# Kernel optimization log

Measured on AMD Instinct MI355X. Metric: run time of the kernel, lower is better.

## Reference

```python
import jax, jax.numpy as jnp
import numpy as np

N_HEADS = 4
N_CLASS = 20
REL_PATTERN = [(5, 3)]
DIF_PATTERN = [(3, 6)]


def im2col(x, ksize, dilation):
    # x: (N,C,H,W) -> (C, ksize*ksize, H*W*N); last dim flattened in (h,w,n) order,
    # matching the torch im2col_indices / permute(1,2,3,0) layout used by the module.
    N, C, H, W = x.shape
    p = (ksize // 2) * dilation
    xp = jnp.pad(x, ((0, 0), (0, 0), (p, p), (p, p)))
    cols = jnp.stack([xp[:, :, fi * dilation:fi * dilation + H, fj * dilation:fj * dilation + W]
                      for fi in range(ksize) for fj in range(ksize)], axis=2)  # (N,C,K2,H,W)
    return cols.transpose(1, 2, 3, 4, 0).reshape(C, ksize * ksize, H * W * N)


def col2im(cols, shape, ksize, dilation):
    # cols: (C*K2, H*W*N) -> scatter-add back to (N,C,H,W) (inverse of im2col).
    N, C, H, W = shape
    p = (ksize // 2) * dilation
    K2 = ksize * ksize
    c = cols.reshape(C, K2, H, W, N).transpose(4, 0, 1, 2, 3)  # (N,C,K2,H,W)
    out = jnp.zeros((N, C, H + 2 * p, W + 2 * p), cols.dtype)
    k = 0
    for fi in range(ksize):
        for fj in range(ksize):
            out = out.at[:, :, fi * dilation:fi * dilation + H, fj * dilation:fj * dilation + W].add(c[:, :, k])
            k += 1
    return out[:, :, p:p + H, p:p + W]


def gap_pred(x, w):
    hm = jnp.einsum('nchw,kc->nhwk', x, w)  # heatmaps
    return hm.reshape(x.shape[0], -1, hm.shape[-1]).mean(1), hm


def make_mask(heatmaps, label):
    N, H, W, _ = heatmaps.shape
    sm = jax.nn.relu(heatmaps)
    m = jnp.take_along_axis(sm, label[:, None, None, None], axis=3)[..., 0]  # (N,H,W)
    mx = jnp.clip(m.reshape(N, -1).max(1), 1.0, None)
    return jax.lax.stop_gradient((m / mx[:, None, None])[:, None])  # (N,1,H,W), detached


def infusion(V, Kc, Qc, ksize, dilation, n_heads):
    N, Dv, H, W = V.shape
    D = Kc.shape[1]
    h_dim, vh_dim, K2 = D // n_heads, Dv // n_heads, ksize * ksize
    L = H * W * N
    Kt = im2col(Kc, ksize, dilation).reshape(n_heads, h_dim, K2, L)
    Qt = Qc.transpose(1, 2, 3, 0).reshape(n_heads, h_dim, L)
    att = jax.nn.softmax(jnp.einsum('ahkl,ahl->akl', Kt, Qt), axis=1)  # softmax over window
    Vt = im2col(V, ksize, dilation).reshape(n_heads, vh_dim, K2, L)
    out = jnp.einsum('avkl,akl->avl', Vt, att).reshape(Dv, H, W, N)
    return out.transpose(3, 0, 1, 2)


def diffusion(V, Kc, Qc, ksize, dilation, mask, n_heads):
    N, Dv, H, W = V.shape
    D = Kc.shape[1]
    h_dim, vh_dim, K2 = D // n_heads, Dv // n_heads, ksize * ksize
    L = H * W * N
    Kt = im2col(Kc, ksize, dilation).reshape(n_heads, h_dim, K2, L)
    Qt = Qc.transpose(1, 2, 3, 0).reshape(n_heads, h_dim, L)
    att = jax.nn.softmax(jnp.einsum('ahkl,ahl->akl', Kt, Qt), axis=1)
    mflat = mask[:, 0].transpose(1, 2, 0).reshape(-1)  # (H*W*N)
    att = att * mflat[None, None, :]
    Vt = V.transpose(1, 2, 3, 0).reshape(n_heads, vh_dim, L)
    Vcols = (Vt[:, :, None, :] * att[:, None, :, :]).reshape(Dv * K2, L)
    return col2im(Vcols, V.shape, ksize, dilation)


def setup_inputs() -> dict:
    key = jax.random.key(0)
    ks = jax.random.split(key, 8)
    N, C, H, W = 4, 256, 64, 64
    return {
        'feats': jax.random.normal(ks[0], (N, C, H, W), jnp.float32),
        'K': jax.random.normal(ks[1], (N, C, H, W), jnp.float32),
        'Q': jax.random.normal(ks[2], (N, C, H, W), jnp.float32),
        'w_gap': jax.random.normal(ks[3], (N_CLASS, C), jnp.float32) * 0.05,
        'w_gap_r': jax.random.normal(ks[4], (N_CLASS, C), jnp.float32) * 0.05,
        'conv_w': jax.random.normal(ks[5], (C, 2 * C, 3, 3), jnp.float32) * 0.02,
        'conv_b': jax.random.normal(ks[6], (C,), jnp.float32) * 0.02,
        'label': jax.random.randint(ks[7], (N,), 0, N_CLASS),
    }


def reference(feats, K, Q, w_gap, w_gap_r, conv_w, conv_b, label):
    pred, hm = gap_pred(feats, w_gap)
    mask = make_mask(hm, label)
    # NOTE: Bayes calls infuse(feats, Q, K, ...) with K/Q swapped vs the Infusion signature.
    feats_r = sum(infusion(feats, Q, K, ksz, dil, N_HEADS) for ksz, dil in REL_PATTERN)
    pred_r, _ = gap_pred(feats_r, w_gap_r)
    feats_d = sum(diffusion(feats, K, Q, ksz, dil, mask, N_HEADS) for ksz, dil in DIF_PATTERN)
    x = jnp.concatenate([feats * mask, feats_d], axis=1)
    nxt = jax.lax.conv_general_dilated(x, conv_w, (1, 1), ((1, 1), (1, 1)),
                                       dimension_numbers=('NCHW', 'OIHW', 'NCHW'))
    nxt = nxt + conv_b[None, :, None, None]
    return nxt, pred, pred_r
```

## Files before the change

kernel.cpp:

```cpp
#include <hip/hip_runtime.h>
#include <hip/hip_bf16.h>

#define N_IMG 4
#define C_CH 256
#define H_DIM 64
#define W_DIM 64
#define HW 4096
#define NCLASS 20
#define NHEADS 4
#define HD 64

typedef __attribute__((ext_vector_type(8))) short short8;
typedef __attribute__((ext_vector_type(4))) float f32x4;

__device__ __forceinline__ ushort f2bf(float f) {
    unsigned u = __float_as_uint(f);
    u += 0x7FFFu + ((u >> 16) & 1u);
    return (ushort)(u >> 16);
}

__global__ __launch_bounds__(256) void k_phaseA(
    ushort* __restrict__ xinp,
    const float* __restrict__ feats, const float* __restrict__ wgap,
    const int* __restrict__ label,
    float* __restrict__ mask, unsigned* __restrict__ mmax,
    float* __restrict__ S_f,
    const float* __restrict__ patch_t,
    const float* __restrict__ center_t,
    float* __restrict__ att_inf,
    const float* __restrict__ cw, ushort* __restrict__ wt3) {
    __shared__ __align__(16) float smem[1600];
    int b = blockIdx.x;
    int t = threadIdx.x;

    if (b < 1040) {
        int n = b / 260, seg = b % 260;
        size_t base;
        if (seg < 66)       base = ((size_t)(n * 66 + 0) * 66 + seg) * 512;
        else if (seg < 132) base = ((size_t)(n * 66 + 65) * 66 + (seg - 66)) * 512;
        else {
            int c = seg - 132;
            int r = 1 + (c >> 1), x = (c & 1) ? 65 : 0;
            base = ((size_t)(n * 66 + r) * 66 + x) * 512;
        }
        ((unsigned*)(xinp + base))[t] = 0u;
    } else if (b < 1296) {
        int bb = b - 1040;
        int n = bb >> 6, h = bb & 63;
        int w = t & 63, cq = t >> 6;
        float* wrow = smem;
        float* part = smem + 256;
        int lab = label[n];
        wrow[t] = wgap[lab * C_CH + t];
        __syncthreads();
        const float* fp = feats + ((size_t)(n * C_CH + cq * 64)) * HW + h * W_DIM + w;
        float acc = 0.f;
        for (int c = 0; c < 64; c++) acc += fp[(size_t)c * HW] * wrow[cq * 64 + c];
        part[cq * 64 + w] = acc;
        __syncthreads();
        if (cq == 0) {
            float m = fmaxf(part[w] + part[64 + w] + part[128 + w] + part[192 + w], 0.f);
            mask[n * HW + h * W_DIM + w] = m;
            for (int off = 32; off; off >>= 1) m = fmaxf(m, __shfl_down(m, off, 64));
            if (w == 0) atomicMax(&mmax[n], __float_as_uint(m));
        }
    } else if (b < 2320) {
        int nc = b - 1296;
        const float* p = feats + (size_t)nc * HW;
        float s = 0.f;
        for (int i = t; i < HW; i += 256) s += p[i];
        float* red = smem;
        for (int off = 32; off; off >>= 1) s += __shfl_down(s, off, 64);
        int wid = t >> 6;
        if ((t & 63) == 0) red[wid] = s;
        __syncthreads();
        if (t == 0) S_f[nc] = red[0] + red[1] + red[2] + red[3];
    } else if (b < 3344) {
        int idx = b - 2320;
        int a = idx >> 8;
        int bb = idx & 255;
        int n = bb >> 6, h = bb & 63;
        int w = t & 63;
        int kq = t >> 6;
        float* att_s = smem;

        int k0 = (kq == 0) ? 0 : (1 + kq * 6);
        int nk = (kq == 0) ? 7 : 6;
        int offc[7]; float msk[7];
#pragma unroll
        for (int j = 0; j < 7; j++) {
            int k = k0 + ((j < nk) ? j : 0);
            int y = h + (k / 5 - 2) * 3, x = w + (k % 5 - 2) * 3;
            bool v = (y >= 0 && y < 64 && x >= 0 && x < 64) && (j < nk);
            offc[j] = v ? y * 64 + x : 0;
            msk[j] = v ? 1.f : 0.f;
        }
        float s[7];
#pragma unroll
        for (int j = 0; j < 7; j++) s[j] = 0.f;
        const float* cp = center_t + ((size_t)(n * C_CH + a * HD)) * HW + h * W_DIM + w;
        const float* pp = patch_t + ((size_t)(n * C_CH + a * HD)) * HW;
        for (int c4 = 0; c4 < 64; c4 += 4) {
            float cen[4];
            float pv[4][7];
#pragma unroll
            for (int u = 0; u < 4; u++)
                cen[u] = cp[(size_t)(c4 + u) * HW];
#pragma unroll
            for (int u = 0; u < 4; u++) {
                const float* pc = pp + (size_t)(c4 + u) * HW;
#pragma unroll
                for (int j = 0; j < 7; j++)
                    if (j < nk) pv[u][j] = pc[offc[j]];
            }
#pragma unroll
            for (int u = 0; u < 4; u++)
#pragma unroll
                for (int j = 0; j < 7; j++)
                    if (j < nk) s[j] += pv[u][j] * msk[j] * cen[u];
        }
#pragma unroll
        for (int j = 0; j < 7; j++)
            if (j < nk) att_s[(k0 + j) * 64 + w] = s[j];
        __syncthreads();
        if (t < 64) {
            float v[25];
            float mx = -1e30f;
#pragma unroll
            for (int k = 0; k < 25; k++) { v[k] = att_s[k * 64 + t]; mx = fmaxf(mx, v[k]); }
            float sum = 0.f;
#pragma unroll
            for (int k = 0; k < 25; k++) { v[k] = __expf(v[k] - mx); sum += v[k]; }
            float inv = 1.0f / sum;
#pragma unroll
            for (int k = 0; k < 25; k++)
                att_inf[((size_t)(a * 25 + k) * N_IMG + n) * HW + h * 64 + t] = v[k] * inv;
        }
    } else {
        int idx = (b - 3344) * 256 + t;
        const float* p = cw + (size_t)idx * 9;
        int ic = idx & 511;
        int oc = idx >> 9;
        int icc = ic >> 5, lq = (ic & 31) >> 3, pos = ic & 7;
#pragma unroll
        for (int kk = 0; kk < 9; kk++)
            wt3[((((size_t)(icc * 9 + kk)) * 4 + lq) * 256 + oc) * 8 + pos] = f2bf(p[kk]);
    }
}

__global__ __launch_bounds__(1024) void k_phaseB(
    const float* __restrict__ patch_t,
    const float* __restrict__ center_t,
    const float* __restrict__ mask, const unsigned* __restrict__ mmax,
    float* __restrict__ att_dif,
    const float* __restrict__ att_inf, float* __restrict__ Wpl) {
    __shared__ float att_s[4][9][64];
    int b = blockIdx.x;
    int t = threadIdx.x;

    if (b < 256) {
        int n = b >> 6, h = b & 63;
        int w = t & 63;
        int a = (t >> 6) & 3;
        int cq = t >> 8;
        for (int i = t; i < 4 * 9 * 64; i += 1024) ((float*)att_s)[i] = 0.f;
        __syncthreads();
        int off[9];
#pragma unroll
        for (int k = 0; k < 9; k++) {
            int y = h + (k / 3 - 1) * 6, x = w + (k % 3 - 1) * 6;
            off[k] = (y >= 0 && y < 64 && x >= 0 && x < 64) ? y * 64 + x : -1;
        }
        float s[9];
#pragma unroll
        for (int k = 0; k < 9; k++) s[k] = 0.f;
        const float* cp = center_t + ((size_t)(n * C_CH + a * HD + cq * 16)) * HW + h * W_DIM + w;
        const float* pp = patch_t + ((size_t)(n * C_CH + a * HD + cq * 16)) * HW;
        for (int c = 0; c < 16; c++) {
            float cen = cp[(size_t)c * HW];
            const float* pc = pp + (size_t)c * HW;
#pragma unroll
            for (int k = 0; k < 9; k++) {
                float pv = (off[k] >= 0) ? pc[off[k]] : 0.f;
                s[k] += pv * cen;
            }
        }
#pragma unroll
        for (int k = 0; k < 9; k++) atomicAdd(&att_s[a][k][w], s[k]);
        __syncthreads();
        if (cq == 0) {
            float v[9];
            float mx = -1e30f;
#pragma unroll
            for (int k = 0; k < 9; k++) { v[k] = att_s[a][k][w]; mx = fmaxf(mx, v[k]); }
            float sum = 0.f;
#pragma unroll
            for (int k = 0; k < 9; k++) { v[k] = __expf(v[k] - mx); sum += v[k]; }
            float mnorm = fmaxf(__uint_as_float(mmax[n]), 1.0f);
            float mm = (mask[n * HW + h * W_DIM + w] / mnorm) / sum;
#pragma unroll
            for (int k = 0; k < 9; k++)
                att_dif[((size_t)(a * 9 + k) * N_IMG + n) * HW + h * W_DIM + w] = v[k] * mm;
        }
    } else {
        int b2 = b - 256;
        int x = t & 63, a = (t >> 6) & 3, yl = t >> 8;
        int row = b2 * 4 + yl;
        int n = row >> 6, y = row & 63;
        float s = 0.f;
#pragma unroll
        for (int k = 0; k < 25; k++) {
            int sy = y - (k / 5 - 2) * 3, sx = x - (k % 5 - 2) * 3;
            if (sy >= 0 && sy < 64 && sx >= 0 && sx < 64)
                s += att_inf[((size_t)(a * 25 + k) * N_IMG + n) * HW + sy * 64 + sx];
        }
        Wpl[((size_t)a * N_IMG + n) * HW + y * 64 + x] = s;
    }
}

__global__ __launch_bounds__(256) void k_phaseC(
    const float* __restrict__ feats, const float* __restrict__ Wpl,
    float* __restrict__ S_r,
    const float* __restrict__ mask, const unsigned* __restrict__ mmax,
    const float* __restrict__ att, ushort* __restrict__ xinp) {
    __shared__ __align__(16) char smemc[31488];
    int b = blockIdx.x;
    int t = threadIdx.x;

    if (b < 1024) {
        int nc = b;
        int n = nc >> 8, c = nc & 255;
        int a = c >> 6;
        const f32x4* p4 = (const f32x4*)(feats + (size_t)nc * HW);
        const f32x4* w4 = (const f32x4*)(Wpl + ((size_t)a * N_IMG + n) * HW);
        f32x4 a4 = (f32x4){0.f, 0.f, 0.f, 0.f};
        for (int i = t; i < HW / 4; i += 256) {
            f32x4 u = p4[i], v = w4[i];
            a4 += u * v;
        }
        float s = a4[0] + a4[1] + a4[2] + a4[3];
        float* red = (float*)smemc;
        for (int off = 32; off; off >>= 1) s += __shfl_down(s, off, 64);
        int wid = t >> 6;
        if ((t & 63) == 0) red[wid] = s;
        __syncthreads();
        if (t == 0) S_r[nc] = red[0] + red[1] + red[2] + red[3];
    } else {
        int idx = b - 1024;
        int y = idx & 63, n = (idx >> 6) & 3, g = idx >> 8;
        int x = t & 63, cg = t >> 6;
        float (*ftile)[32][64] = (float(*)[32][64])smemc;
        float (*att_s)[64]     = (float(*)[64])(smemc + 24576);
        ushort (*sx)[36]       = (ushort(*)[36])(smemc + 26880);
        short8 pk;
        if (g < 8) {
            int cbase = g * 32 + cg * 8;
            float mnorm = fmaxf(__uint_as_float(mmax[n]), 1.0f);
            float mval = mask[n * HW + y * 64 + x] / mnorm;
            const float* fp = feats + ((size_t)(n * C_CH + cbase)) * HW + y * 64 + x;
            float v[8];
#pragma unroll
            for (int i = 0; i < 8; i++) v[i] = fp[(size_t)i * HW];
#pragma unroll
            for (int i = 0; i < 8; i++) pk[i] = (short)f2bf(v[i] * mval);
        } else {
            int gd = g - 8;
            int a = gd >> 1;
            int cd = gd * 32;
            for (int idx2 = t; idx2 < 9 * 64; idx2 += 256) {
                int k = idx2 >> 6, w = idx2 & 63;
                int sy = y - (k / 3 - 1) * 6;
                att_s[k][w] = (sy >= 0 && sy < 64)
                    ? att[((size_t)(a * 9 + k) * N_IMG + n) * HW + sy * 64 + w] : 0.f;
            }
            const float* fb = feats + ((size_t)(n * C_CH + cd)) * HW;
#pragma unroll
            for (int i = 0; i < 24; i++) {
                int idx2 = t + 256 * i;
                int r = idx2 >> 11, c = (idx2 >> 6) & 31, xx = idx2 & 63;
                int ry = y + (r - 1) * 6;
                ((float*)ftile)[idx2] = (ry >= 0 && ry < 64)
                    ? fb[(size_t)c * HW + ry * 64 + xx] : 0.f;
            }
            __syncthreads();
#pragma unroll
            for (int cl = 0; cl < 8; cl++) {
                int c = cg * 8 + cl;
                float v = 0.f;
#pragma unroll
                for (int k = 0; k < 9; k++) {
                    int sxk = x - (k % 3 - 1) * 6;
                    if (sxk >= 0 && sxk < 64)
                        v += ftile[2 - k / 3][c][sxk] * att_s[k][sxk];
                }
                pk[cl] = (short)f2bf(v);
            }
        }
        __syncthreads();
        *(short8*)&sx[x][cg * 8] = pk;
        __syncthreads();
        int px = t >> 2, j = t & 3;
        short8 v8 = *(const short8*)&sx[px][j * 8];
        int chb = (g < 8) ? g * 32 : 256 + (g - 8) * 32;
        *(short8*)(xinp + ((size_t)((n * 66 + y + 1) * 66 + px + 1)) * 512 + chb + j * 8) = v8;
    }
}

#define LDS_PXW 32
__global__ __launch_bounds__(512, 4) void k_conv_mfma(
    const ushort* __restrict__ xinp,
    const ushort* __restrict__ wt3,
    const float* __restrict__ cb,
    float* __restrict__ out,
    const float* __restrict__ S_f, const float* __restrict__ wg,
    const float* __restrict__ S_r, const float* __restrict__ wgr,
    float* __restrict__ pred_out) {
    int bid = blockIdx.x;
    if (bid == 512) {
        int idx = threadIdx.x;
        if (idx < N_IMG * NCLASS) {
            int n = idx / NCLASS, k = idx % NCLASS;
            float s = 0.f;
            for (int c = 0; c < C_CH; c++) s += wg[k * C_CH + c] * S_f[n * C_CH + c];
            pred_out[idx] = s * (1.0f / HW);
        } else if (idx < 2 * N_IMG * NCLASS) {
            int j = idx - N_IMG * NCLASS;
            int n = j / NCLASS, k = j % NCLASS;
            float s = 0.f;
            for (int c = 0; c < C_CH; c++) s += wgr[k * C_CH + c] * S_r[n * C_CH + c];
            pred_out[idx] = s * (1.0f / HW);
        }
        return;
    }
    int t512 = threadIdx.x;
    int half = t512 >> 8;
    int th   = t512 & 255;
    int lane = t512 & 63;
    int wid  = (t512 >> 6) & 3;
    int w   = (bid & 7) * 64 + (bid >> 3);
    int och = w & 1;
    int y0  = (w >> 1) & 63;
    int n   = w >> 7;
    int ocw = och * 128 + wid * 32;
    int l15 = lane & 15, lq = lane >> 4;

    __shared__ ushort lds[2][2][792 * 8];

    f32x4 acc[2][4];
#pragma unroll
    for (int m = 0; m < 2; m++)
#pragma unroll
        for (int xs = 0; xs < 4; xs++) acc[m][xs] = (f32x4){0.f, 0.f, 0.f, 0.f};

    int s0 = th, s1 = th + 256, s2 = th + 512, s3 = th + 768;
    short8 g0, g1, g2, g3;
    int icb = half * 8;

#define SWZ_OFF(R, PX, J) (((((((R) * 66 + (PX)) << 2) | (J)) ^ ((PX) & 7)) << 3))

#define STAGE_LOAD(ICC)                                                              \
    {                                                                                \
        int icc_ = (ICC);                                                            \
        { int r = s0 / 264, rem = s0 % 264, px = rem >> 2, j = rem & 3;              \
          g0 = *(const short8*)(xinp + ((size_t)((n * 66 + y0 + r) * 66 + px)) * 512 \
                                 + icc_ * 32 + j * 8); }                             \
        { int r = s1 / 264, rem = s1 % 264, px = rem >> 2, j = rem & 3;              \
          g1 = *(const short8*)(xinp + ((size_t)((n * 66 + y0 + r) * 66 + px)) * 512 \
                                 + icc_ * 32 + j * 8); }                             \
        { int r = s2 / 264, rem = s2 % 264, px = rem >> 2, j = rem & 3;              \
          g2 = *(const short8*)(xinp + ((size_t)((n * 66 + y0 + r) * 66 + px)) * 512 \
                                 + icc_ * 32 + j * 8); }                             \
        if (s3 < 792) {                                                              \
          int r = s3 / 264, rem = s3 % 264, px = rem >> 2, j = rem & 3;              \
          g3 = *(const short8*)(xinp + ((size_t)((n * 66 + y0 + r) * 66 + px)) * 512 \
                                 + icc_ * 32 + j * 8); }                             \
    }

#define STAGE_WRITE(BUF)                                                             \
    {                                                                                \
        ushort* lb = &lds[half][BUF][0];                                             \
        { int r = s0 / 264, rem = s0 % 264, px = rem >> 2, j = rem & 3;              \
          *(short8*)&lb[SWZ_OFF(r, px, j)] = g0; }                                   \
        { int r = s1 / 264, rem = s1 % 264, px = rem >> 2, j = rem & 3;              \
          *(short8*)&lb[SWZ_OFF(r, px, j)] = g1; }                                   \
        { int r = s2 / 264, rem = s2 % 264, px = rem >> 2, j = rem & 3;              \
          *(short8*)&lb[SWZ_OFF(r, px, j)] = g2; }                                   \
        if (s3 < 792) {                                                              \
          int r = s3 / 264, rem = s3 % 264, px = rem >> 2, j = rem & 3;              \
          *(short8*)&lb[SWZ_OFF(r, px, j)] = g3; }                                   \
    }

    STAGE_LOAD(icb);
    STAGE_WRITE(0);
    __syncthreads();

    int cur = 0;
    for (int it = 0; it < 8; it++) {
        int icc = icb + it;
        if (it < 7) STAGE_LOAD(icc + 1);
        const ushort* lp = &lds[half][cur][0];
        const ushort* am0 = wt3 + (size_t)icc * 73728 + lq * 2048 + (ocw + l15) * 8;
        const ushort* am1 = am0 + 128;
        short8 a0c = *(const short8*)(am0);
        short8 a1c = *(const short8*)(am1);
        short8 a0n = *(const short8*)(am0 + 8192);
        short8 a1n = *(const short8*)(am1 + 8192);
#pragma unroll
        for (int kk = 0; kk < 9; kk++) {
            short8 a0nn, a1nn;
            if (kk < 7) {
                a0nn = *(const short8*)(am0 + (kk + 2) * 8192);
                a1nn = *(const short8*)(am1 + (kk + 2) * 8192);
            }
            int ky = kk / 3, kx = kk % 3;
            int kxl = kx + l15;
            const ushort* lrow = lp + SWZ_OFF(ky, kxl, lq);
            short8 b0 = *(const short8*)(lrow);
            short8 b1 = *(const short8*)(lrow + 16 * LDS_PXW);
            short8 b2 = *(const short8*)(lrow + 32 * LDS_PXW);
            short8 b3 = *(const short8*)(lrow + 48 * LDS_PXW);
            acc[0][0] = __builtin_amdgcn_mfma_f32_16x16x32_bf16(a0c, b0, acc[0][0], 0, 0, 0);
            acc[1][0] = __builtin_amdgcn_mfma_f32_16x16x32_bf16(a1c, b0, acc[1][0], 0, 0, 0);
            acc[0][1] = __builtin_amdgcn_mfma_f32_16x16x32_bf16(a0c, b1, acc[0][1], 0, 0, 0);
            acc[1][1] = __builtin_amdgcn_mfma_f32_16x16x32_bf16(a1c, b1, acc[1][1], 0, 0, 0);
            acc[0][2] = __builtin_amdgcn_mfma_f32_16x16x32_bf16(a0c, b2, acc[0][2], 0, 0, 0);
            acc[1][2] = __builtin_amdgcn_mfma_f32_16x16x32_bf16(a1c, b2, acc[1][2], 0, 0, 0);
            acc[0][3] = __builtin_amdgcn_mfma_f32_16x16x32_bf16(a0c, b3, acc[0][3], 0, 0, 0);
            acc[1][3] = __builtin_amdgcn_mfma_f32_16x16x32_bf16(a1c, b3, acc[1][3], 0, 0, 0);
            a0c = a0n; a1c = a1n; a0n = a0nn; a1n = a1nn;
        }
        if (it < 7) {
            STAGE_WRITE(cur ^ 1);
            __syncthreads();
            cur ^= 1;
        }
    }

    float* red = (float*)&lds[0][0][0];
    __syncthreads();
    if (half == 1) {
#pragma unroll
        for (int m = 0; m < 2; m++)
#pragma unroll
            for (int xs = 0; xs < 4; xs++)
#pragma unroll
                for (int r = 0; r < 4; r++)
                    red[(((m * 4 + xs) * 4) + r) * 256 + th] = acc[m][xs][r];
    }
    __syncthreads();
    if (half == 0) {
#pragma unroll
        for (int m = 0; m < 2; m++) {
#pragma unroll
            for (int r = 0; r < 4; r++) {
                int oc = ocw + m * 16 + lq * 4 + r;
                float bias = cb[oc];
                float* op = out + ((size_t)(n * 256 + oc)) * HW + y0 * 64 + l15;
#pragma unroll
                for (int xs = 0; xs < 4; xs++)
                    op[xs * 16] = acc[m][xs][r] + red[(((m * 4 + xs) * 4) + r) * 256 + th] + bias;
            }
        }
    }
#undef STAGE_LOAD
#undef STAGE_WRITE
#undef SWZ_OFF
}

extern "C" void kernel_launch(void* const* d_in, const int* in_sizes, int n_in,
                              void* d_out, int out_size, void* d_ws, size_t ws_size,
                              hipStream_t stream) {
    const float* feats  = (const float*)d_in[0];
    const float* Kten   = (const float*)d_in[1];
    const float* Qten   = (const float*)d_in[2];
    const float* w_gap  = (const float*)d_in[3];
    const float* w_gapr = (const float*)d_in[4];
    const float* conv_w = (const float*)d_in[5];
    const float* conv_b = (const float*)d_in[6];
    const int*   label  = (const int*)d_in[7];
    float* ob           = (float*)d_out;

    float* ws = (float*)d_ws;
    float*    mask    = ws;
    unsigned* mmax    = (unsigned*)(ws + 16384);
    float*    S_f     = ws + 16384 + 4;
    float*    S_r     = S_f + 1024;
    float*    att_inf = S_r + 1024;
    float*    Wpl     = att_inf + 1638400;
    float*    att_dif = Wpl + 65536;
    ushort*   xinp    = (ushort*)(att_dif + 589824);
    ushort*   wt3     = xinp + 8921088;

    const int NXT = N_IMG * C_CH * HW;

    hipMemsetAsync(mmax, 0, N_IMG * sizeof(unsigned), stream);

    k_phaseA<<<3856, 256, 0, stream>>>(xinp, feats, w_gap, label, mask, mmax,
                                       S_f, Qten, Kten, att_inf, conv_w, wt3);
    k_phaseB<<<320, 1024, 0, stream>>>(Kten, Qten, mask, mmax, att_dif,
                                       att_inf, Wpl);
    k_phaseC<<<5120, 256, 0, stream>>>(feats, Wpl, S_r, mask, mmax, att_dif, xinp);

    k_conv_mfma<<<513, 512, 0, stream>>>(xinp, wt3, conv_b, ob,
                                         S_f, w_gap, S_r, w_gapr, ob + NXT);
}
```

Measured before the change: 148.9 us.

## Move diffusion attention into phase A and defer mask scaling to phase C

After: 143.5 us, median of 2. 1.04x faster.

```diff
diff --git a/kernel.cpp b/kernel.cpp
--- a/kernel.cpp
+++ b/kernel.cpp
@@ -25,16 +25,122 @@
     const int* __restrict__ label,
     float* __restrict__ mask, unsigned* __restrict__ mmax,
     float* __restrict__ S_f,
-    const float* __restrict__ patch_t,
-    const float* __restrict__ center_t,
-    float* __restrict__ att_inf,
+    const float* __restrict__ Kten, const float* __restrict__ Qten,
+    float* __restrict__ att_inf, float* __restrict__ att_dif,
     const float* __restrict__ cw, ushort* __restrict__ wt3) {
     __shared__ __align__(16) float smem[1600];
     int b = blockIdx.x;
     int t = threadIdx.x;
 
-    if (b < 1040) {
-        int n = b / 260, seg = b % 260;
+    if (b < 1024) {
+        int a = b >> 8;
+        int bb = b & 255;
+        int n = bb >> 6, h = bb & 63;
+        int w = t & 63;
+        int kq = t >> 6;
+        float* att_s = smem;
+
+        int k0 = (kq == 0) ? 0 : (1 + kq * 6);
+        int nk = (kq == 0) ? 7 : 6;
+        int offc[7]; float msk[7];
+#pragma unroll
+        for (int j = 0; j < 7; j++) {
+            int k = k0 + ((j < nk) ? j : 0);
+            int y = h + (k / 5 - 2) * 3, x = w + (k % 5 - 2) * 3;
+            bool v = (y >= 0 && y < 64 && x >= 0 && x < 64) && (j < nk);
+            offc[j] = v ? y * 64 + x : 0;
+            msk[j] = v ? 1.f : 0.f;
+        }
+        float s[7];
+#pragma unroll
+        for (int j = 0; j < 7; j++) s[j] = 0.f;
+        const float* cp = Kten + ((size_t)(n * C_CH + a * HD)) * HW + h * W_DIM + w;
+        const float* pp = Qten + ((size_t)(n * C_CH + a * HD)) * HW;
+        for (int c4 = 0; c4 < 64; c4 += 4) {
+            float cen[4];
+            float pv[4][7];
+#pragma unroll
+            for (int u = 0; u < 4; u++)
+                cen[u] = cp[(size_t)(c4 + u) * HW];
+#pragma unroll
+            for (int u = 0; u < 4; u++) {
+                const float* pc = pp + (size_t)(c4 + u) * HW;
+#pragma unroll
+                for (int j = 0; j < 7; j++)
+                    if (j < nk) pv[u][j] = pc[offc[j]];
+            }
+#pragma unroll
+            for (int u = 0; u < 4; u++)
+#pragma unroll
+                for (int j = 0; j < 7; j++)
+                    if (j < nk) s[j] += pv[u][j] * msk[j] * cen[u];
+        }
+#pragma unroll
+        for (int j = 0; j < 7; j++)
+            if (j < nk) att_s[(k0 + j) * 64 + w] = s[j];
+        __syncthreads();
+        if (t < 64) {
+            float v[25];
+            float mx = -1e30f;
+#pragma unroll
+            for (int k = 0; k < 25; k++) { v[k] = att_s[k * 64 + t]; mx = fmaxf(mx, v[k]); }
+            float sum = 0.f;
+#pragma unroll
+            for (int k = 0; k < 25; k++) { v[k] = __expf(v[k] - mx); sum += v[k]; }
+            float inv = 1.0f / sum;
+#pragma unroll
+            for (int k = 0; k < 25; k++)
+                att_inf[((size_t)(a * 25 + k) * N_IMG + n) * HW + h * 64 + t] = v[k] * inv;
+        }
+    } else if (b < 1280) {
+        int bb = b - 1024;
+        int n = bb >> 6, h = bb & 63;
+        int w = t & 63, a = t >> 6;
+        int offc[9]; float msk[9];
+#pragma unroll
+        for (int k = 0; k < 9; k++) {
+            int y = h + (k / 3 - 1) * 6, x = w + (k % 3 - 1) * 6;
+            bool v = (y >= 0 && y < 64 && x >= 0 && x < 64);
+            offc[k] = v ? y * 64 + x : 0;
+            msk[k] = v ? 1.f : 0.f;
+        }
+        float s[9];
+#pragma unroll
+        for (int k = 0; k < 9; k++) s[k] = 0.f;
+        const float* cp = Qten + ((size_t)(n * C_CH + a * HD)) * HW + h * W_DIM + w;
+        const float* pp = Kten + ((size_t)(n * C_CH + a * HD)) * HW;
+        for (int c4 = 0; c4 < 64; c4 += 4) {
+            float cen[4];
+            float pv[4][9];
+#pragma unroll
+            for (int u = 0; u < 4; u++)
+                cen[u] = cp[(size_t)(c4 + u) * HW];
+#pragma unroll
+            for (int u = 0; u < 4; u++) {
+                const float* pc = pp + (size_t)(c4 + u) * HW;
+#pragma unroll
+                for (int k = 0; k < 9; k++)
+                    pv[u][k] = pc[offc[k]];
+            }
+#pragma unroll
+            for (int u = 0; u < 4; u++)
+#pragma unroll
+                for (int k = 0; k < 9; k++)
+                    s[k] += pv[u][k] * msk[k] * cen[u];
+        }
+        float mx = -1e30f;
+#pragma unroll
+        for (int k = 0; k < 9; k++) mx = fmaxf(mx, s[k]);
+        float sum = 0.f;
+#pragma unroll
+        for (int k = 0; k < 9; k++) { s[k] = __expf(s[k] - mx); sum += s[k]; }
+        float inv = 1.0f / sum;
+#pragma unroll
+        for (int k = 0; k < 9; k++)
+            att_dif[((size_t)(a * 9 + k) * N_IMG + n) * HW + h * W_DIM + w] = s[k] * inv;
+    } else if (b < 2320) {
+        int bb = b - 1280;
+        int n = bb / 260, seg = bb % 260;
         size_t base;
         if (seg < 66)       base = ((size_t)(n * 66 + 0) * 66 + seg) * 512;
         else if (seg < 132) base = ((size_t)(n * 66 + 65) * 66 + (seg - 66)) * 512;
@@ -44,8 +150,8 @@
             base = ((size_t)(n * 66 + r) * 66 + x) * 512;
         }
         ((unsigned*)(xinp + base))[t] = 0u;
-    } else if (b < 1296) {
-        int bb = b - 1040;
+    } else if (b < 2576) {
+        int bb = b - 2320;
         int n = bb >> 6, h = bb & 63;
         int w = t & 63, cq = t >> 6;
         float* wrow = smem;
@@ -64,8 +170,8 @@
             for (int off = 32; off; off >>= 1) m = fmaxf(m, __shfl_down(m, off, 64));
             if (w == 0) atomicMax(&mmax[n], __float_as_uint(m));
         }
-    } else if (b < 2320) {
-        int nc = b - 1296;
+    } else if (b < 3600) {
+        int nc = b - 2576;
         const float* p = feats + (size_t)nc * HW;
         float s = 0.f;
         for (int i = t; i < HW; i += 256) s += p[i];
@@ -75,69 +181,8 @@
         if ((t & 63) == 0) red[wid] = s;
         __syncthreads();
         if (t == 0) S_f[nc] = red[0] + red[1] + red[2] + red[3];
-    } else if (b < 3344) {
-        int idx = b - 2320;
-        int a = idx >> 8;
-        int bb = idx & 255;
-        int n = bb >> 6, h = bb & 63;
-        int w = t & 63;
-        int kq = t >> 6;
-        float* att_s = smem;
-
-        int k0 = (kq == 0) ? 0 : (1 + kq * 6);
-        int nk = (kq == 0) ? 7 : 6;
-        int offc[7]; float msk[7];
-#pragma unroll
-        for (int j = 0; j < 7; j++) {
-            int k = k0 + ((j < nk) ? j : 0);
-            int y = h + (k / 5 - 2) * 3, x = w + (k % 5 - 2) * 3;
-            bool v = (y >= 0 && y < 64 && x >= 0 && x < 64) && (j < nk);
-            offc[j] = v ? y * 64 + x : 0;
-            msk[j] = v ? 1.f : 0.f;
-        }
-        float s[7];
-#pragma unroll
-        for (int j = 0; j < 7; j++) s[j] = 0.f;
-        const float* cp = center_t + ((size_t)(n * C_CH + a * HD)) * HW + h * W_DIM + w;
-        const float* pp = patch_t + ((size_t)(n * C_CH + a * HD)) * HW;
-        for (int c4 = 0; c4 < 64; c4 += 4) {
-            float cen[4];
-            float pv[4][7];
-#pragma unroll
-            for (int u = 0; u < 4; u++)
-                cen[u] = cp[(size_t)(c4 + u) * HW];
-#pragma unroll
-            for (int u = 0; u < 4; u++) {
-                const float* pc = pp + (size_t)(c4 + u) * HW;
-#pragma unroll
-                for (int j = 0; j < 7; j++)
-                    if (j < nk) pv[u][j] = pc[offc[j]];
-            }
-#pragma unroll
-            for (int u = 0; u < 4; u++)
-#pragma unroll
-                for (int j = 0; j < 7; j++)
-                    if (j < nk) s[j] += pv[u][j] * msk[j] * cen[u];
-        }
-#pragma unroll
-        for (int j = 0; j < 7; j++)
-            if (j < nk) att_s[(k0 + j) * 64 + w] = s[j];
-        __syncthreads();
-        if (t < 64) {
-            float v[25];
-            float mx = -1e30f;
-#pragma unroll
-            for (int k = 0; k < 25; k++) { v[k] = att_s[k * 64 + t]; mx = fmaxf(mx, v[k]); }
-            float sum = 0.f;
-#pragma unroll
-            for (int k = 0; k < 25; k++) { v[k] = __expf(v[k] - mx); sum += v[k]; }
-            float inv = 1.0f / sum;
-#pragma unroll
-            for (int k = 0; k < 25; k++)
-                att_inf[((size_t)(a * 25 + k) * N_IMG + n) * HW + h * 64 + t] = v[k] * inv;
-        }
     } else {
-        int idx = (b - 3344) * 256 + t;
+        int idx = (b - 3600) * 256 + t;
         const float* p = cw + (size_t)idx * 9;
         int ic = idx & 511;
         int oc = idx >> 9;
@@ -148,74 +193,20 @@
     }
 }
 
-__global__ __launch_bounds__(1024) void k_phaseB(
-    const float* __restrict__ patch_t,
-    const float* __restrict__ center_t,
-    const float* __restrict__ mask, const unsigned* __restrict__ mmax,
-    float* __restrict__ att_dif,
-    const float* __restrict__ att_inf, float* __restrict__ Wpl) {
-    __shared__ float att_s[4][9][64];
+__global__ __launch_bounds__(256) void k_scatter_w(const float* __restrict__ att,
+                                                   float* __restrict__ W) {
     int b = blockIdx.x;
+    int n = b >> 6, y = b & 63;
     int t = threadIdx.x;
-
-    if (b < 256) {
-        int n = b >> 6, h = b & 63;
-        int w = t & 63;
-        int a = (t >> 6) & 3;
-        int cq = t >> 8;
-        for (int i = t; i < 4 * 9 * 64; i += 1024) ((float*)att_s)[i] = 0.f;
-        __syncthreads();
-        int off[9];
-#pragma unroll
-        for (int k = 0; k < 9; k++) {
-            int y = h + (k / 3 - 1) * 6, x = w + (k % 3 - 1) * 6;
-            off[k] = (y >= 0 && y < 64 && x >= 0 && x < 64) ? y * 64 + x : -1;
-        }
-        float s[9];
-#pragma unroll
-        for (int k = 0; k < 9; k++) s[k] = 0.f;
-        const float* cp = center_t + ((size_t)(n * C_CH + a * HD + cq * 16)) * HW + h * W_DIM + w;
-        const float* pp = patch_t + ((size_t)(n * C_CH + a * HD + cq * 16)) * HW;
-        for (int c = 0; c < 16; c++) {
-            float cen = cp[(size_t)c * HW];
-            const float* pc = pp + (size_t)c * HW;
-#pragma unroll
-            for (int k = 0; k < 9; k++) {
-                float pv = (off[k] >= 0) ? pc[off[k]] : 0.f;
-                s[k] += pv * cen;
-            }
-        }
-#pragma unroll
-        for (int k = 0; k < 9; k++) atomicAdd(&att_s[a][k][w], s[k]);
-        __syncthreads();
-        if (cq == 0) {
-            float v[9];
-            float mx = -1e30f;
-#pragma unroll
-            for (int k = 0; k < 9; k++) { v[k] = att_s[a][k][w]; mx = fmaxf(mx, v[k]); }
-            float sum = 0.f;
-#pragma unroll
-            for (int k = 0; k < 9; k++) { v[k] = __expf(v[k] - mx); sum += v[k]; }
-            float mnorm = fmaxf(__uint_as_float(mmax[n]), 1.0f);
-            float mm = (mask[n * HW + h * W_DIM + w] / mnorm) / sum;
-#pragma unroll
-            for (int k = 0; k < 9; k++)
-                att_dif[((size_t)(a * 9 + k) * N_IMG + n) * HW + h * W_DIM + w] = v[k] * mm;
-        }
-    } else {
-        int b2 = b - 256;
-        int x = t & 63, a = (t >> 6) & 3, yl = t >> 8;
-        int row = b2 * 4 + yl;
-        int n = row >> 6, y = row & 63;
-        float s = 0.f;
-#pragma unroll
-        for (int k = 0; k < 25; k++) {
-            int sy = y - (k / 5 - 2) * 3, sx = x - (k % 5 - 2) * 3;
-            if (sy >= 0 && sy < 64 && sx >= 0 && sx < 64)
-                s += att_inf[((size_t)(a * 25 + k) * N_IMG + n) * HW + sy * 64 + sx];
-        }
-        Wpl[((size_t)a * N_IMG + n) * HW + y * 64 + x] = s;
-    }
+    int x = t & 63, a = t >> 6;
+    float s = 0.f;
+#pragma unroll
+    for (int k = 0; k < 25; k++) {
+        int sy = y - (k / 5 - 2) * 3, sx = x - (k % 5 - 2) * 3;
+        if (sy >= 0 && sy < 64 && sx >= 0 && sx < 64)
+            s += att[((size_t)(a * 25 + k) * N_IMG + n) * HW + sy * 64 + sx];
+    }
+    W[((size_t)a * N_IMG + n) * HW + y * 64 + x] = s;
 }
 
 __global__ __launch_bounds__(256) void k_phaseC(
@@ -267,11 +258,15 @@
             int gd = g - 8;
             int a = gd >> 1;
             int cd = gd * 32;
+            float mnorm = fmaxf(__uint_as_float(mmax[n]), 1.0f);
+            float rmn = 1.0f / mnorm;
             for (int idx2 = t; idx2 < 9 * 64; idx2 += 256) {
                 int k = idx2 >> 6, w = idx2 & 63;
                 int sy = y - (k / 3 - 1) * 6;
                 att_s[k][w] = (sy >= 0 && sy < 64)
-                    ? att[((size_t)(a * 9 + k) * N_IMG + n) * HW + sy * 64 + w] : 0.f;
+                    ? att[((size_t)(a * 9 + k) * N_IMG + n) * HW + sy * 64 + w]
+                      * (mask[n * HW + sy * 64 + w] * rmn)
+                    : 0.f;
             }
             const float* fb = feats + ((size_t)(n * C_CH + cd)) * HW;
 #pragma unroll
@@ -306,37 +301,36 @@
     }
 }
 
+__global__ void k_pred2(const float* __restrict__ S_f, const float* __restrict__ wg,
+                        const float* __restrict__ S_r, const float* __restrict__ wgr,
+                        float* __restrict__ out) {
+    int idx = threadIdx.x;
+    if (idx < N_IMG * NCLASS) {
+        int n = idx / NCLASS, k = idx % NCLASS;
+        float s = 0.f;
+        for (int c = 0; c < C_CH; c++) s += wg[k * C_CH + c] * S_f[n * C_CH + c];
+        out[idx] = s * (1.0f / HW);
+    } else if (idx < 2 * N_IMG * NCLASS) {
+        int j = idx - N_IMG * NCLASS;
+        int n = j / NCLASS, k = j % NCLASS;
+        float s = 0.f;
+        for (int c = 0; c < C_CH; c++) s += wgr[k * C_CH + c] * S_r[n * C_CH + c];
+        out[idx] = s * (1.0f / HW);
+    }
+}
+
 #define LDS_PXW 32
 __global__ __launch_bounds__(512, 4) void k_conv_mfma(
     const ushort* __restrict__ xinp,
     const ushort* __restrict__ wt3,
     const float* __restrict__ cb,
-    float* __restrict__ out,
-    const float* __restrict__ S_f, const float* __restrict__ wg,
-    const float* __restrict__ S_r, const float* __restrict__ wgr,
-    float* __restrict__ pred_out) {
-    int bid = blockIdx.x;
-    if (bid == 512) {
-        int idx = threadIdx.x;
-        if (idx < N_IMG * NCLASS) {
-            int n = idx / NCLASS, k = idx % NCLASS;
-            float s = 0.f;
-            for (int c = 0; c < C_CH; c++) s += wg[k * C_CH + c] * S_f[n * C_CH + c];
-            pred_out[idx] = s * (1.0f / HW);
-        } else if (idx < 2 * N_IMG * NCLASS) {
-            int j = idx - N_IMG * NCLASS;
-            int n = j / NCLASS, k = j % NCLASS;
-            float s = 0.f;
-            for (int c = 0; c < C_CH; c++) s += wgr[k * C_CH + c] * S_r[n * C_CH + c];
-            pred_out[idx] = s * (1.0f / HW);
-        }
-        return;
-    }
+    float* __restrict__ out) {
     int t512 = threadIdx.x;
     int half = t512 >> 8;
     int th   = t512 & 255;
     int lane = t512 & 63;
     int wid  = (t512 >> 6) & 3;
+    int bid = blockIdx.x;
     int w   = (bid & 7) * 64 + (bid >> 3);
     int och = w & 1;
     int y0  = (w >> 1) & 63;
@@ -495,12 +489,12 @@
 
     hipMemsetAsync(mmax, 0, N_IMG * sizeof(unsigned), stream);
 
-    k_phaseA<<<3856, 256, 0, stream>>>(xinp, feats, w_gap, label, mask, mmax,
-                                       S_f, Qten, Kten, att_inf, conv_w, wt3);
-    k_phaseB<<<320, 1024, 0, stream>>>(Kten, Qten, mask, mmax, att_dif,
-                                       att_inf, Wpl);
+    k_phaseA<<<4112, 256, 0, stream>>>(xinp, feats, w_gap, label, mask, mmax,
+                                       S_f, Kten, Qten, att_inf, att_dif,
+                                       conv_w, wt3);
+    k_scatter_w<<<N_IMG * H_DIM, 256, 0, stream>>>(att_inf, Wpl);
     k_phaseC<<<5120, 256, 0, stream>>>(feats, Wpl, S_r, mask, mmax, att_dif, xinp);
 
-    k_conv_mfma<<<513, 512, 0, stream>>>(xinp, wt3, conv_b, ob,
-                                         S_f, w_gap, S_r, w_gapr, ob + NXT);
-}
+    k_conv_mfma<<<512, 512, 0, stream>>>(xinp, wt3, conv_b, ob);
+    k_pred2<<<1, 192, 0, stream>>>(S_f, w_gap, S_r, w_gapr, ob + NXT);
+}
```
